# Kernel optimization log

Measured on AMD Instinct MI355X. Metric: run time of the kernel, lower is better.

## Reference

```python
import jax, jax.numpy as jnp
import numpy as np

NUM_JOINTS = 75
COORDS = 3
HIDDEN = 256
MID = HIDDEN // 2
LN_EPS = 1e-5


def build_adjacency_matrix(num_joints=NUM_JOINTS):
    edges = []
    hand_bones = [(0, 1), (1, 2), (2, 3), (3, 4), (0, 5), (5, 6), (6, 7), (7, 8), (0, 9), (9, 10), (10, 11), (11, 12), (0, 13), (13, 14), (14, 15), (15, 16), (0, 17), (17, 18), (18, 19), (19, 20), (5, 9), (9, 13), (13, 17)]
    for i, j in hand_bones:
        edges.extend([(i, j), (j, i)])
    for i, j in hand_bones:
        edges.extend([(i + 21, j + 21), (j + 21, i + 21)])
    pose_bones = [(0, 1), (1, 2), (2, 3), (3, 7), (0, 4), (4, 5), (5, 6), (6, 8), (9, 10), (11, 12), (11, 13), (13, 15), (12, 14), (14, 16), (11, 23), (12, 24), (23, 24), (23, 25), (25, 27), (27, 29), (29, 31), (24, 26), (26, 28), (28, 30), (30, 32), (15, 17), (15, 19), (15, 21), (16, 18), (16, 20), (16, 22)]
    off = 42
    for i, j in pose_bones:
        if i < 33 and j < 33:
            edges.extend([(i + off, j + off), (j + off, i + off)])
    edges.extend([(57, 0), (0, 57), (58, 21), (21, 58)])
    A = np.zeros((num_joints, num_joints), dtype=np.float32)
    np.fill_diagonal(A, 1.0)
    for i, j in edges:
        if i < num_joints and j < num_joints:
            A[i, j] = 1.0
    deg = A.sum(axis=1)
    d = np.where(deg > 0, deg ** -0.5, 0.0).astype(np.float32)
    return (d[:, None] * A) * d[None, :]


def setup_inputs() -> dict:
    key = jax.random.key(0)
    ks = jax.random.split(key, 8)
    B = 16384
    x = jax.random.normal(ks[0], (B, NUM_JOINTS, COORDS), dtype=jnp.float32)
    A = jnp.asarray(build_adjacency_matrix())
    # Kaiming-uniform style init scales (values only need to be plausible)
    W1 = jax.random.normal(ks[1], (MID, COORDS), dtype=jnp.float32) * (1.0 / np.sqrt(COORDS))
    g1 = jnp.ones((MID,), jnp.float32)
    b1 = jnp.zeros((MID,), jnp.float32)
    W2 = jax.random.normal(ks[2], (HIDDEN, MID), dtype=jnp.float32) * (1.0 / np.sqrt(MID))
    g2 = jnp.ones((HIDDEN,), jnp.float32)
    b2 = jnp.zeros((HIDDEN,), jnp.float32)
    Wp = jax.random.normal(ks[3], (HIDDEN, COORDS), dtype=jnp.float32) * (1.0 / np.sqrt(COORDS))
    bp = jnp.zeros((HIDDEN,), jnp.float32)
    return {"x": x, "A": A, "W1": W1, "g1": g1, "b1": b1, "W2": W2, "g2": g2, "b2": b2, "Wp": Wp, "bp": bp}


def _layer_norm(h, gamma, beta):
    mu = h.mean(axis=-1, keepdims=True)
    var = ((h - mu) ** 2).mean(axis=-1, keepdims=True)
    return (h - mu) * jax.lax.rsqrt(var + LN_EPS) * gamma + beta


def _gcn(x, A, W, gamma, beta):
    # Z = A @ X @ W^T, then LayerNorm, then ReLU
    h = jnp.einsum('ij,bjc->bic', A, x)
    h = jnp.einsum('bic,oc->bio', h, W)
    return jax.nn.relu(_layer_norm(h, gamma, beta))


def reference(x, A, W1, g1, b1, W2, g2, b2, Wp, bp):
    # skip: per-frame mean of a linear projection of raw coords
    skip = (jnp.einsum('bjc,oc->bjo', x, Wp) + bp).mean(axis=1)  # (B, H)
    h = _gcn(x, A, W1, g1, b1)    # (B, 75, 128)
    h = _gcn(h, A, W2, g2, b2)    # (B, 75, 256)
    return h.mean(axis=1) + skip  # (B, 256)
```

## Files before the change

kernel.cpp:

```cpp
#include <hip/hip_runtime.h>

typedef __bf16 bf16;
typedef __bf16 bf16x4 __attribute__((ext_vector_type(4)));
typedef __bf16 bf16x8 __attribute__((ext_vector_type(8)));
typedef float  f32x2  __attribute__((ext_vector_type(2)));
typedef float  f32x4  __attribute__((ext_vector_type(4)));
typedef unsigned int u32;
typedef u32 u32x2 __attribute__((ext_vector_type(2)));
typedef u32 u32x4 __attribute__((ext_vector_type(4)));
typedef unsigned short u16;

#define NJ 75
#define SA 104
#define SH 88
#define SG 136
#define SX 104
#define LN_EPS 1e-5f
#define MFMA16(a,b,c) __builtin_amdgcn_mfma_f32_16x16x32_bf16((a),(b),(c),0,0,0)

static __device__ __forceinline__ f32x4 f4z(){ f32x4 v={0.f,0.f,0.f,0.f}; return v; }
static __device__ __forceinline__ u32 pk2(float a, float b){
  u32 ua = (u32)__builtin_bit_cast(u16,(bf16)a);
  u32 ub = (u32)__builtin_bit_cast(u16,(bf16)b);
  return ua | (ub<<16);
}
static __device__ __forceinline__ float lo16f(u32 u){ return __uint_as_float(u<<16); }
static __device__ __forceinline__ float hi16f(u32 u){ return __uint_as_float(u & 0xffff0000u); }

template<int C>
static __device__ __forceinline__ float dppterm(float v){
  return __int_as_float(__builtin_amdgcn_update_dpp(0, __float_as_int(v), C, 0xF, 0xF, true));
}
static __device__ __forceinline__ float red16(float v){
  v += dppterm<0xB1>(v);
  v += dppterm<0x4E>(v);
  v += dppterm<0x141>(v);
  v += dppterm<0x140>(v);
  return v;
}

__global__ __launch_bounds__(512, 4)
void ke11(const float* __restrict__ gx,  const float* __restrict__ gA,
          const float* __restrict__ gW1, const float* __restrict__ gg1, const float* __restrict__ gb1,
          const float* __restrict__ gW2, const float* __restrict__ gg2, const float* __restrict__ gb2,
          const float* __restrict__ gWp, const float* __restrict__ gbp,
          float* __restrict__ gout, int B)
{
  __shared__ __align__(16) bf16 A_lds[80*SA];
  __shared__ __align__(16) bf16 h1[128*SH + 16];
  __shared__ __align__(16) bf16 gss[80*SG];
  __shared__ __align__(16) bf16 xT[4*SX];
  __shared__ __align__(16) float red2[16*80*2];
  __shared__ __align__(16) float fin[80*2];
  __shared__ __align__(16) float skl[4][256];
  __shared__ __align__(16) float b1l[128];
  __shared__ __align__(16) u32  g2b2[256];
  __shared__ __align__(16) bf16 W1l4[128*4];
  __shared__ __align__(16) u32x2 wpl[256];
  __shared__ __align__(16) float Msh[12];
  __shared__ float xbars[4];

  const int tid = threadIdx.x;
  const int w   = tid >> 6;
  const int l   = tid & 63;
  const int l16 = l & 15;
  const int lg  = l >> 4;

  for (int i = tid; i < 80*SA; i += 512) {
    const int r = i / SA, c = i - r*SA;
    A_lds[i] = (bf16)((r < NJ && c < NJ) ? gA[r*NJ + c] : 0.f);
  }
  for (int i = tid; i < 128*SH + 16; i += 512) h1[i] = (bf16)0.f;
  for (int i = tid; i < 4*SX; i += 512) xT[i] = (bf16)0.f;
  float* wsc = red2;
  if (tid < 128) {
    wsc[tid*3+0] = gW1[tid*3+0];
    wsc[tid*3+1] = gW1[tid*3+1];
    wsc[tid*3+2] = gW1[tid*3+2];
    b1l[tid] = gb1[tid];
    fin[tid] = gg1[tid];
  }
  if (tid < 256) {
    g2b2[tid] = pk2(gg2[tid], gb2[tid]);
    u32x2 wv = { pk2(gWp[tid*3+0], gWp[tid*3+1]), pk2(gWp[tid*3+2], gbp[tid]) };
    wpl[tid] = wv;
  }
  __syncthreads();
  if (tid < 3) {
    float s = 0.f;
    for (int c = 0; c < 128; ++c) s += wsc[c*3 + tid];
    Msh[6 + tid] = s * (1.f/128.f);
  }
  __syncthreads();
  if (tid < 128) {
    float wt0 = wsc[tid*3+0] - Msh[6];
    float wt1 = wsc[tid*3+1] - Msh[7];
    float wt2 = wsc[tid*3+2] - Msh[8];
    const float g1v = fin[tid];
    W1l4[tid*4+0] = (bf16)(g1v*wt0);
    W1l4[tid*4+1] = (bf16)(g1v*wt1);
    W1l4[tid*4+2] = (bf16)(g1v*wt2);
    W1l4[tid*4+3] = (bf16)0.f;
    wsc[tid*3+0] = wt0; wsc[tid*3+1] = wt1; wsc[tid*3+2] = wt2;
  }
  __syncthreads();
  if (tid < 6) {
    const int pa[6] = {0,1,2,0,0,1};
    const int pb[6] = {0,1,2,1,2,2};
    float s = 0.f;
    for (int c = 0; c < 128; ++c) s += wsc[c*3 + pa[tid]] * wsc[c*3 + pb[tid]];
    Msh[tid] = s * (1.f/128.f);
  }

  bf16x8 W2fr[2][4];
  #pragma unroll
  for (int ot = 0; ot < 2; ++ot) {
    const int o = 16*(2*w + ot) + l16;
    #pragma unroll
    for (int ks = 0; ks < 4; ++ks) {
      bf16x8 v;
      #pragma unroll
      for (int e = 0; e < 8; ++e) v[e] = (bf16)gW2[o*128 + 32*ks + 8*lg + e];
      W2fr[ot][ks] = v;
    }
  }
  __syncthreads();
  const float M00 = Msh[0], M11 = Msh[1], M22 = Msh[2];
  const float M01 = Msh[3], M02 = Msh[4], M12 = Msh[5];

  const int  fpb  = (B + 511) >> 9;
  const long base = (long)blockIdx.x * fpb;

  float xv[4] = {0.f, 0.f, 0.f, 0.f};
  if (w == 5) {
    long fg = base; if (fg >= B) fg = B - 1;
    #pragma unroll
    for (int k = 0; k < 4; ++k) { const int t = l + 64*k; if (t < 225) xv[k] = gx[fg*225 + t]; }
  }
  __syncthreads();

  f32x4 zacc[5][2];
  #pragma unroll
  for (int jt = 0; jt < 5; ++jt) { zacc[jt][0] = f4z(); zacc[jt][1] = f4z(); }

  const int nint = fpb + 2;
  for (int i = 0; i < nint; ++i) {
    if (i >= 1 && i <= fpb) {
      const bf16* hb = &h1[(16*w + l16)*SH];
      bf16x8 hf0 = *(const bf16x8*)&hb[ 0 + 8*lg];
      bf16x8 hf1 = *(const bf16x8*)&hb[32 + 8*lg];
      bf16x8 hf2 = *(const bf16x8*)&hb[64 + 8*lg];
      #pragma unroll
      for (int jt = 0; jt < 5; ++jt) {
        const bf16* ab = &A_lds[(16*jt + l16)*SA + 8*lg];
        f32x4 ag = f4z();
        ag = MFMA16(hf0, *(const bf16x8*)&ab[ 0], ag);
        ag = MFMA16(hf1, *(const bf16x8*)&ab[32], ag);
        ag = MFMA16(hf2, *(const bf16x8*)&ab[64], ag);
        bf16x4 p;
        #pragma unroll
        for (int r = 0; r < 4; ++r) p[r] = (bf16)ag[r];
        *(bf16x4*)&gss[(16*jt + l16)*SG + 16*w + 4*lg] = p;
      }
    }
    if (w == 5 && i < fpb) {
      float s0 = 0.f, s1 = 0.f, s2 = 0.f;
      #pragma unroll
      for (int k = 0; k < 4; ++k) {
        const int t = l + 64*k;
        if (t < 225) {
          const int j = (t*21846) >> 16;
          const int co = t - 3*j;
          xT[co*SX + j] = (bf16)xv[k];
          if (co == 0) s0 += xv[k]; else if (co == 1) s1 += xv[k]; else s2 += xv[k];
        }
      }
      s0 = red16(s0); s0 += __shfl_xor(s0, 16); s0 += __shfl_xor(s0, 32);
      s1 = red16(s1); s1 += __shfl_xor(s1, 16); s1 += __shfl_xor(s1, 32);
      s2 = red16(s2); s2 += __shfl_xor(s2, 16); s2 += __shfl_xor(s2, 32);
      if (l == 0) { xbars[0] = s0*(1.f/NJ); xbars[1] = s1*(1.f/NJ); xbars[2] = s2*(1.f/NJ); }
    }
    if (w == 6 && i >= 2) {
      float S = 0.f, Q = 0.f;
      #pragma unroll
      for (int slot = 0; slot < 16; ++slot) {
        const f32x2 a = *(const f32x2*)&red2[(slot*80 + l)*2];
        S += a[0]; Q += a[1];
      }
      const float mu = S * (1.f/256.f);
      const float rs = rsqrtf(Q * (1.f/256.f) - mu*mu + LN_EPS);
      f32x2 nr = { -mu*rs, rs };
      *(f32x2*)&fin[l*2] = nr;
    }
    if (w == 7 && i >= 2 && l < 16) {
      const int j2 = 64 + l;
      float S = 0.f, Q = 0.f;
      #pragma unroll
      for (int slot = 0; slot < 16; ++slot) {
        const f32x2 a = *(const f32x2*)&red2[(slot*80 + j2)*2];
        S += a[0]; Q += a[1];
      }
      const float mu = S * (1.f/256.f);
      const float rs = rsqrtf(Q * (1.f/256.f) - mu*mu + LN_EPS);
      f32x2 nr = { -mu*rs, rs };
      *(f32x2*)&fin[j2*2] = nr;
    }
    __syncthreads();

    if (i >= 2) {
      float nmv[5], rsv[5];
      #pragma unroll
      for (int jt = 0; jt < 5; ++jt) {
        const f32x2 nr = *(const f32x2*)&fin[(16*jt + l16)*2];
        nmv[jt] = nr[0]; rsv[jt] = nr[1];
      }
      float os[2][4];
      #pragma unroll
      for (int ot = 0; ot < 2; ++ot) {
        const u32x4 gb = *(const u32x4*)&g2b2[16*(2*w + ot) + 4*lg];
        #pragma unroll
        for (int r = 0; r < 4; ++r) os[ot][r] = 0.f;
        #pragma unroll
        for (int jt = 0; jt < 5; ++jt) {
          #pragma unroll
          for (int r = 0; r < 4; ++r) {
            float v = fmaf(fmaf(zacc[jt][ot][r], rsv[jt], nmv[jt]), lo16f(gb[r]), hi16f(gb[r]));
            v = fmaxf(v, 0.f);
            if (jt == 4) v = (l16 < 11) ? v : 0.f;
            os[ot][r] += v;
          }
        }
        #pragma unroll
        for (int r = 0; r < 4; ++r) os[ot][r] = red16(os[ot][r]);
      }
      const long f = base + (i - 2);
      if (l16 == 0 && f < B) {
        #pragma unroll
        for (int ot = 0; ot < 2; ++ot) {
          const int o0 = 16*(2*w + ot) + 4*lg;
          const f32x4 sk = *(const f32x4*)&skl[(i-2)&3][o0];
          f32x4 res;
          #pragma unroll
          for (int r = 0; r < 4; ++r) res[r] = os[ot][r]*(1.f/NJ) + sk[r];
          *(f32x4*)&gout[f*256 + o0] = res;
        }
      }
    }
    if (i >= 1 && i <= fpb) {
      #pragma unroll
      for (int jt = 0; jt < 5; ++jt) {
        const bf16* gr = &gss[(16*jt + l16)*SG + 8*lg];
        f32x4 z0 = f4z(), z1 = f4z();
        #pragma unroll
        for (int ks = 0; ks < 4; ++ks) {
          const bf16x8 gf = *(const bf16x8*)&gr[32*ks];
          z0 = MFMA16(W2fr[0][ks], gf, z0);
          z1 = MFMA16(W2fr[1][ks], gf, z1);
        }
        float s = 0.f, q = 0.f;
        #pragma unroll
        for (int r = 0; r < 4; ++r) {
          s += z0[r] + z1[r];
          q = fmaf(z0[r], z0[r], q); q = fmaf(z1[r], z1[r], q);
        }
        s += __shfl_xor(s, 16); q += __shfl_xor(q, 16);
        if ((lg & 1) == 0) {
          const int slot = 2*w + (lg >> 1);
          f32x2 sq = {s, q};
          *(f32x2*)&red2[(slot*80 + 16*jt + l16)*2] = sq;
        }
        zacc[jt][0] = z0; zacc[jt][1] = z1;
      }
    }
    if (i < fpb && w < 5) {
      const int xrow = (l16 < 3) ? l16 : 3;
      const bf16* xb = &xT[xrow*SX + 8*lg];
      const bf16* ab = &A_lds[(16*w + l16)*SA + 8*lg];
      f32x4 at = f4z();
      at = MFMA16(*(const bf16x8*)&xb[ 0], *(const bf16x8*)&ab[ 0], at);
      at = MFMA16(*(const bf16x8*)&xb[32], *(const bf16x8*)&ab[32], at);
      at = MFMA16(*(const bf16x8*)&xb[64], *(const bf16x8*)&ab[64], at);
      const float a0 = at[0], a1 = at[1], a2 = at[2];
      float qd = fmaf(M00*a0, a0, fmaf(M11*a1, a1, fmaf(M22*a2, a2, LN_EPS)));
      qd = fmaf(2.f*M01*a0, a1, fmaf(2.f*M02*a0, a2, fmaf(2.f*M12*a1, a2, qd)));
      const float rs = rsqrtf(qd);
      bf16x8 hA;
      #pragma unroll
      for (int e = 0; e < 8; ++e) hA[e] = (bf16)0.f;
      hA[0] = (bf16)((lg == 0) ? a0*rs : 0.f);
      hA[1] = (bf16)((lg == 0) ? a1*rs : 0.f);
      hA[2] = (bf16)((lg == 0) ? a2*rs : 0.f);
      #pragma unroll
      for (int nt = 0; nt < 8; ++nt) {
        const bf16x4 w4 = *(const bf16x4*)&W1l4[(16*nt + l16)*4];
        bf16x8 wb;
        wb[0] = w4[0]; wb[1] = w4[1]; wb[2] = w4[2]; wb[3] = w4[3];
        wb[4] = w4[3]; wb[5] = w4[3]; wb[6] = w4[3]; wb[7] = w4[3];
        const f32x4 hp = MFMA16(hA, wb, f4z());
        const float b1v = b1l[16*nt + l16];
        bf16x4 pkk;
        #pragma unroll
        for (int r = 0; r < 4; ++r) pkk[r] = (bf16)fmaxf(hp[r] + b1v, 0.f);
        *(bf16x4*)&h1[(16*nt + l16)*SH + 16*w + 4*lg] = pkk;
      }
    }
    if (w == 5 && i + 1 < fpb) {
      long fg = base + i + 1; if (fg >= B) fg = B - 1;
      #pragma unroll
      for (int k = 0; k < 4; ++k) { const int t = l + 64*k; if (t < 225) xv[k] = gx[fg*225 + t]; }
    }
    if (w == 6 && i < fpb) {
      const float xb0 = xbars[0], xb1 = xbars[1], xb2 = xbars[2];
      #pragma unroll
      for (int k = 0; k < 4; ++k) {
        const int o = l + 64*k;
        const u32x2 wv = wpl[o];
        skl[i&3][o] = fmaf(lo16f(wv[0]), xb0, fmaf(hi16f(wv[0]), xb1, fmaf(lo16f(wv[1]), xb2, hi16f(wv[1]))));
      }
    }
    __syncthreads();
  }
}

extern "C" void kernel_launch(void* const* d_in, const int* in_sizes, int n_in,
                              void* d_out, int out_size, void* d_ws, size_t ws_size,
                              hipStream_t stream) {
  const float* x  = (const float*)d_in[0];
  const float* A  = (const float*)d_in[1];
  const float* W1 = (const float*)d_in[2];
  const float* g1 = (const float*)d_in[3];
  const float* b1 = (const float*)d_in[4];
  const float* W2 = (const float*)d_in[5];
  const float* g2 = (const float*)d_in[6];
  const float* b2 = (const float*)d_in[7];
  const float* Wp = (const float*)d_in[8];
  const float* bp = (const float*)d_in[9];
  float* out = (float*)d_out;
  const int B = in_sizes[0] / 225;
  ke11<<<dim3(512), dim3(512), 0, stream>>>(x, A, W1, g1, b1, W2, g2, b2, Wp, bp, out, B);
}
```

Baseline: 247.0 us.

## Double-buffer transposed input tile and prefetch frames two iterations ahead

The x transpose and per-frame coordinate mean now happen one iteration early into a double-buffered xTs/xbars, and the global load of x is issued two frames ahead. This takes the load-wait and transpose off the critical path of the layer-1 MFMA wave in each iteration. The skip buffer ring shrinks from 4 to 3 slots, indexed modulo 3. The layer-2 MFMA section is also wrapped in s_setprio to raise those waves' scheduling priority. It costs a little more LDS and keeps loaded frame values live in registers longer.

```diff
diff --git a/kernel.cpp b/kernel.cpp
--- a/kernel.cpp
+++ b/kernel.cpp
@@ -40,7 +40,7 @@
 }
 
 __global__ __launch_bounds__(512, 4)
-void ke11(const float* __restrict__ gx,  const float* __restrict__ gA,
+void ke12(const float* __restrict__ gx,  const float* __restrict__ gA,
           const float* __restrict__ gW1, const float* __restrict__ gg1, const float* __restrict__ gb1,
           const float* __restrict__ gW2, const float* __restrict__ gg2, const float* __restrict__ gb2,
           const float* __restrict__ gWp, const float* __restrict__ gbp,
@@ -49,16 +49,16 @@
   __shared__ __align__(16) bf16 A_lds[80*SA];
   __shared__ __align__(16) bf16 h1[128*SH + 16];
   __shared__ __align__(16) bf16 gss[80*SG];
-  __shared__ __align__(16) bf16 xT[4*SX];
+  __shared__ __align__(16) bf16 xTs[2][4*SX];
   __shared__ __align__(16) float red2[16*80*2];
   __shared__ __align__(16) float fin[80*2];
-  __shared__ __align__(16) float skl[4][256];
+  __shared__ __align__(16) float skl[3][256];
   __shared__ __align__(16) float b1l[128];
   __shared__ __align__(16) u32  g2b2[256];
   __shared__ __align__(16) bf16 W1l4[128*4];
   __shared__ __align__(16) u32x2 wpl[256];
   __shared__ __align__(16) float Msh[12];
-  __shared__ float xbars[4];
+  __shared__ float xbars[2][4];
 
   const int tid = threadIdx.x;
   const int w   = tid >> 6;
@@ -71,7 +71,7 @@
     A_lds[i] = (bf16)((r < NJ && c < NJ) ? gA[r*NJ + c] : 0.f);
   }
   for (int i = tid; i < 128*SH + 16; i += 512) h1[i] = (bf16)0.f;
-  for (int i = tid; i < 4*SX; i += 512) xT[i] = (bf16)0.f;
+  for (int i = tid; i < 2*4*SX; i += 512) ((bf16*)xTs)[i] = (bf16)0.f;
   float* wsc = red2;
   if (tid < 128) {
     wsc[tid*3+0] = gW1[tid*3+0];
@@ -136,6 +136,26 @@
     long fg = base; if (fg >= B) fg = B - 1;
     #pragma unroll
     for (int k = 0; k < 4; ++k) { const int t = l + 64*k; if (t < 225) xv[k] = gx[fg*225 + t]; }
+    float s0 = 0.f, s1 = 0.f, s2 = 0.f;
+    #pragma unroll
+    for (int k = 0; k < 4; ++k) {
+      const int t = l + 64*k;
+      if (t < 225) {
+        const int j = (t*21846) >> 16;
+        const int co = t - 3*j;
+        xTs[0][co*SX + j] = (bf16)xv[k];
+        if (co == 0) s0 += xv[k]; else if (co == 1) s1 += xv[k]; else s2 += xv[k];
+      }
+    }
+    s0 = red16(s0); s0 += __shfl_xor(s0, 16); s0 += __shfl_xor(s0, 32);
+    s1 = red16(s1); s1 += __shfl_xor(s1, 16); s1 += __shfl_xor(s1, 32);
+    s2 = red16(s2); s2 += __shfl_xor(s2, 16); s2 += __shfl_xor(s2, 32);
+    if (l == 0) { xbars[0][0] = s0*(1.f/NJ); xbars[0][1] = s1*(1.f/NJ); xbars[0][2] = s2*(1.f/NJ); }
+    if (1 < fpb) {
+      long f2 = base + 1; if (f2 >= B) f2 = B - 1;
+      #pragma unroll
+      for (int k = 0; k < 4; ++k) { const int t = l + 64*k; if (t < 225) xv[k] = gx[f2*225 + t]; }
+    }
   }
   __syncthreads();
 
@@ -162,23 +182,6 @@
         for (int r = 0; r < 4; ++r) p[r] = (bf16)ag[r];
         *(bf16x4*)&gss[(16*jt + l16)*SG + 16*w + 4*lg] = p;
       }
-    }
-    if (w == 5 && i < fpb) {
-      float s0 = 0.f, s1 = 0.f, s2 = 0.f;
-      #pragma unroll
-      for (int k = 0; k < 4; ++k) {
-        const int t = l + 64*k;
-        if (t < 225) {
-          const int j = (t*21846) >> 16;
-          const int co = t - 3*j;
-          xT[co*SX + j] = (bf16)xv[k];
-          if (co == 0) s0 += xv[k]; else if (co == 1) s1 += xv[k]; else s2 += xv[k];
-        }
-      }
-      s0 = red16(s0); s0 += __shfl_xor(s0, 16); s0 += __shfl_xor(s0, 32);
-      s1 = red16(s1); s1 += __shfl_xor(s1, 16); s1 += __shfl_xor(s1, 32);
-      s2 = red16(s2); s2 += __shfl_xor(s2, 16); s2 += __shfl_xor(s2, 32);
-      if (l == 0) { xbars[0] = s0*(1.f/NJ); xbars[1] = s1*(1.f/NJ); xbars[2] = s2*(1.f/NJ); }
     }
     if (w == 6 && i >= 2) {
       float S = 0.f, Q = 0.f;
@@ -238,7 +241,7 @@
         #pragma unroll
         for (int ot = 0; ot < 2; ++ot) {
           const int o0 = 16*(2*w + ot) + 4*lg;
-          const f32x4 sk = *(const f32x4*)&skl[(i-2)&3][o0];
+          const f32x4 sk = *(const f32x4*)&skl[(i-2)%3][o0];
           f32x4 res;
           #pragma unroll
           for (int r = 0; r < 4; ++r) res[r] = os[ot][r]*(1.f/NJ) + sk[r];
@@ -247,6 +250,7 @@
       }
     }
     if (i >= 1 && i <= fpb) {
+      __builtin_amdgcn_s_setprio(1);
       #pragma unroll
       for (int jt = 0; jt < 5; ++jt) {
         const bf16* gr = &gss[(16*jt + l16)*SG + 8*lg];
@@ -271,10 +275,11 @@
         }
         zacc[jt][0] = z0; zacc[jt][1] = z1;
       }
+      __builtin_amdgcn_s_setprio(0);
     }
     if (i < fpb && w < 5) {
       const int xrow = (l16 < 3) ? l16 : 3;
-      const bf16* xb = &xT[xrow*SX + 8*lg];
+      const bf16* xb = &xTs[i&1][xrow*SX + 8*lg];
       const bf16* ab = &A_lds[(16*w + l16)*SA + 8*lg];
       f32x4 at = f4z();
       at = MFMA16(*(const bf16x8*)&xb[ 0], *(const bf16x8*)&ab[ 0], at);
@@ -305,17 +310,35 @@
       }
     }
     if (w == 5 && i + 1 < fpb) {
-      long fg = base + i + 1; if (fg >= B) fg = B - 1;
-      #pragma unroll
-      for (int k = 0; k < 4; ++k) { const int t = l + 64*k; if (t < 225) xv[k] = gx[fg*225 + t]; }
+      const int slot = (i+1) & 1;
+      float s0 = 0.f, s1 = 0.f, s2 = 0.f;
+      #pragma unroll
+      for (int k = 0; k < 4; ++k) {
+        const int t = l + 64*k;
+        if (t < 225) {
+          const int j = (t*21846) >> 16;
+          const int co = t - 3*j;
+          xTs[slot][co*SX + j] = (bf16)xv[k];
+          if (co == 0) s0 += xv[k]; else if (co == 1) s1 += xv[k]; else s2 += xv[k];
+        }
+      }
+      s0 = red16(s0); s0 += __shfl_xor(s0, 16); s0 += __shfl_xor(s0, 32);
+      s1 = red16(s1); s1 += __shfl_xor(s1, 16); s1 += __shfl_xor(s1, 32);
+      s2 = red16(s2); s2 += __shfl_xor(s2, 16); s2 += __shfl_xor(s2, 32);
+      if (l == 0) { xbars[slot][0] = s0*(1.f/NJ); xbars[slot][1] = s1*(1.f/NJ); xbars[slot][2] = s2*(1.f/NJ); }
+      if (i + 2 < fpb) {
+        long fg = base + i + 2; if (fg >= B) fg = B - 1;
+        #pragma unroll
+        for (int k = 0; k < 4; ++k) { const int t = l + 64*k; if (t < 225) xv[k] = gx[fg*225 + t]; }
+      }
     }
     if (w == 6 && i < fpb) {
-      const float xb0 = xbars[0], xb1 = xbars[1], xb2 = xbars[2];
+      const float xb0 = xbars[i&1][0], xb1 = xbars[i&1][1], xb2 = xbars[i&1][2];
       #pragma unroll
       for (int k = 0; k < 4; ++k) {
         const int o = l + 64*k;
         const u32x2 wv = wpl[o];
-        skl[i&3][o] = fmaf(lo16f(wv[0]), xb0, fmaf(hi16f(wv[0]), xb1, fmaf(lo16f(wv[1]), xb2, hi16f(wv[1]))));
+        skl[i%3][o] = fmaf(lo16f(wv[0]), xb0, fmaf(hi16f(wv[0]), xb1, fmaf(lo16f(wv[1]), xb2, hi16f(wv[1]))));
       }
     }
     __syncthreads();
@@ -337,5 +360,5 @@
   const float* bp = (const float*)d_in[9];
   float* out = (float*)d_out;
   const int B = in_sizes[0] / 225;
-  ke11<<<dim3(512), dim3(512), 0, stream>>>(x, A, W1, g1, b1, W2, g2, b2, Wp, bp, out, B);
-}
+  ke12<<<dim3(512), dim3(512), 0, stream>>>(x, A, W1, g1, b1, W2, g2, b2, Wp, bp, out, B);
+}
```

Result: no change. 247.7 us (+0.3%).
